# Performance work log

Measured on AMD Instinct MI355X. Metric: run time of the kernel, lower is better.

Reference implementation:

```python
import jax, jax.numpy as jnp
import numpy as np

ALPHA = 1.702   # GLU sigmoid scale
LIMIT = 7.0     # clamp limit
K = 2           # experts per token


def setup_inputs() -> dict:
    key = jax.random.key(0)
    ks = jax.random.split(key, 4)
    B, S, H, E, I = 1, 1024, 1024, 8, 1024
    return {
        "hidden_states": jax.random.normal(ks[0], (B, S, H), jnp.float32),
        "router_weight": jax.random.normal(ks[1], (E, H), jnp.float32),
        "router_bias": jnp.zeros((E,), jnp.float32),
        "gate_up_proj": jax.random.normal(ks[2], (E, H, 2 * I), jnp.float32) * 0.02,
        "gate_up_bias": jnp.zeros((E, 2 * I), jnp.float32),
        "down_proj": jax.random.normal(ks[3], (E, I, H), jnp.float32) * 0.02,
        "down_bias": jnp.zeros((E, H), jnp.float32),
    }


def reference(hidden_states, router_weight, router_bias, gate_up_proj,
              gate_up_bias, down_proj, down_bias):
    B, S, H = hidden_states.shape
    E = router_weight.shape[0]
    I = down_proj.shape[1]
    T = B * S

    flat = hidden_states.reshape(T, H)

    # Router: softmax over experts, top-K selection (weights NOT renormalized).
    logits = flat @ router_weight.T + router_bias               # [T, E]
    scores = jax.nn.softmax(logits, axis=-1)
    topk_vals, topk_idx = jax.lax.top_k(scores, K)              # [T, K]

    # Dense per-token expert weight matrix (equivalent of dispatch metadata +
    # combine * topk_weights in the tt pipeline); top-k indices are unique.
    w = jnp.zeros((T, E), scores.dtype).at[
        jnp.arange(T)[:, None], topk_idx].set(topk_vals)        # [T, E]

    # Expert MLP with clamped GLU (gpt-oss style).
    gu = jnp.einsum('th,ehf->tef', flat, gate_up_proj) + gate_up_bias  # [T,E,2I]
    gate = jnp.minimum(gu[..., :I], LIMIT)
    up = jnp.clip(gu[..., I:], -LIMIT, LIMIT)
    glu = gate * jax.nn.sigmoid(gate * ALPHA)
    act = (up + 1.0) * glu                                       # [T, E, I]

    down = jnp.einsum('tei,eih->teh', act, down_proj) + down_bias  # [T, E, H]

    # Weighted combine over selected experts.
    out = jnp.einsum('teh,te->th', down, w)
    return out.reshape(B, S, H)
```

## Files before the change

kernel.cpp:

```cpp
#include <hip/hip_runtime.h>
#include <hip/hip_bf16.h>


typedef unsigned short u16;
typedef __attribute__((ext_vector_type(8))) __bf16 bf16x8;
typedef __attribute__((ext_vector_type(4))) float f32x4;

#define T_TOK 1024
#define H_DIM 1024
#define E_NUM 8
#define I_DIM 1024
#define ALPHA 1.702f
#define LIMIT 7.0f
#define LSTR 72
#define DPART (2048 * 1024)

__device__ __forceinline__ u16 f2bf(float f) {
    unsigned u = __builtin_bit_cast(unsigned, f);
    u = (u + 0x7FFFu + ((u >> 16) & 1u)) >> 16;
    return (u16)u;
}

__device__ __forceinline__ f32x4 mfma16(bf16x8 a, bf16x8 b, f32x4 c) {
    return __builtin_amdgcn_mfma_f32_16x16x32_bf16(a, b, c, 0, 0, 0);
}

__global__ void k_zero(int* counts) {
    if (threadIdx.x < E_NUM) counts[threadIdx.x] = 0;
}

__global__ __launch_bounds__(256) void k_router(
    const float* __restrict__ x, const float* __restrict__ rw,
    const float* __restrict__ rb,
    int* __restrict__ counts, int* __restrict__ tk_e, int* __restrict__ tk_slot,
    float* __restrict__ tk_w, int* __restrict__ tok_list,
    float* __restrict__ w_list, u16* __restrict__ xb)
{
    const int t = blockIdx.x;
    const int tid = threadIdx.x;
    const float4 xv = *(const float4*)(x + (size_t)t * H_DIM + tid * 4);

    unsigned lo = (unsigned)f2bf(xv.x) | ((unsigned)f2bf(xv.y) << 16);
    unsigned hi = (unsigned)f2bf(xv.z) | ((unsigned)f2bf(xv.w) << 16);
    *(uint2*)(xb + (size_t)t * H_DIM + tid * 4) = make_uint2(lo, hi);

    float p[E_NUM];
#pragma unroll
    for (int e = 0; e < E_NUM; ++e) {
        const float4 wv = *(const float4*)(rw + e * H_DIM + tid * 4);
        p[e] = xv.x * wv.x + xv.y * wv.y + xv.z * wv.z + xv.w * wv.w;
    }
#pragma unroll
    for (int off = 32; off; off >>= 1) {
#pragma unroll
        for (int e = 0; e < E_NUM; ++e) p[e] += __shfl_down(p[e], off, 64);
    }
    __shared__ float red[4][E_NUM];
    const int lane = tid & 63, wvid = tid >> 6;
    if (lane == 0) {
#pragma unroll
        for (int e = 0; e < E_NUM; ++e) red[wvid][e] = p[e];
    }
    __syncthreads();
    if (tid == 0) {
        float lg[E_NUM];
#pragma unroll
        for (int e = 0; e < E_NUM; ++e)
            lg[e] = red[0][e] + red[1][e] + red[2][e] + red[3][e] + rb[e];
        float m1 = -1e30f, m2 = -1e30f; int i1 = 0, i2 = 0;
#pragma unroll
        for (int e = 0; e < E_NUM; ++e) {
            float l = lg[e];
            if (l > m1) { m2 = m1; i2 = i1; m1 = l; i1 = e; }
            else if (l > m2) { m2 = l; i2 = e; }
        }
        float s = 0.f;
#pragma unroll
        for (int e = 0; e < E_NUM; ++e) s += __expf(lg[e] - m1);
        const float w0 = 1.0f / s;
        const float w1 = __expf(m2 - m1) / s;
        int ee[2] = { i1, i2 };
        float ww[2] = { w0, w1 };
#pragma unroll
        for (int k = 0; k < 2; ++k) {
            int e = ee[k];
            int slot = atomicAdd(&counts[e], 1);
            tok_list[e * T_TOK + slot] = t;
            w_list[e * T_TOK + slot] = ww[k];
            tk_e[t * 2 + k] = e;
            tk_slot[t * 2 + k] = slot;
            tk_w[t * 2 + k] = ww[k];
        }
    }
}

__global__ void k_prefix(const int* __restrict__ counts, int* __restrict__ ebase) {
    if (threadIdx.x == 0) {
        int a = 0;
        for (int e = 0; e < E_NUM; ++e) { ebase[e] = a; a += counts[e]; }
    }
}

__global__ __launch_bounds__(256) void k_gateup(
    const float* __restrict__ gup, const float* __restrict__ gub,
    const int* __restrict__ counts, const int* __restrict__ ebase,
    const int* __restrict__ tok_list, const u16* __restrict__ xb,
    u16* __restrict__ act)
{
    const int e = blockIdx.z;
    const int cnt = counts[e];
    const int m0 = blockIdx.y * 64;
    if (m0 >= cnt) return;
    const int n0 = blockIdx.x * 32;
    const int abase = ebase[e];
    const int tid = threadIdx.x;

    __shared__ __align__(16) u16 As[64 * LSTR];
    __shared__ __align__(16) u16 Bs[64 * LSTR];

    const int arow_i = tid >> 2, akq = (tid & 3) * 16;
    const int aslot = m0 + arow_i;
    const int atok = (aslot < cnt) ? tok_list[e * T_TOK + aslot] : 0;
    const u16* asrc = xb + (size_t)atok * H_DIM + akq;
    u16* adst = &As[arow_i * LSTR + akq];

    const int kk = tid >> 2, q = tid & 3;
    const float* bg = gup + ((size_t)e << 21) + n0 + q * 4;
    const float* bu = bg + 1024;

    const int lane = tid & 63, wv = tid >> 6;
    const int fm = lane & 15, kg = lane >> 4;

    f32x4 accg[2], accu[2];
#pragma unroll
    for (int nt = 0; nt < 2; ++nt) {
        accg[nt] = (f32x4){0.f, 0.f, 0.f, 0.f};
        accu[nt] = (f32x4){0.f, 0.f, 0.f, 0.f};
    }

    uint4  pa0, pa1;
    float4 pg0, pg1, pu0, pu1;
    {
        pa0 = *(const uint4*)(asrc);
        pa1 = *(const uint4*)(asrc + 8);
        const float* g = bg + (size_t)kk * 2048;
        const float* u = bu + (size_t)kk * 2048;
        pg0 = *(const float4*)(g);      pg1 = *(const float4*)(g + 16);
        pu0 = *(const float4*)(u);      pu1 = *(const float4*)(u + 16);
    }

    for (int kb = 0; kb < H_DIM; kb += 64) {
        __syncthreads();
        *(uint4*)adst       = pa0;
        *(uint4*)(adst + 8) = pa1;
        {
            const float* g0 = (const float*)&pg0; const float* g1 = (const float*)&pg1;
            const float* u0 = (const float*)&pu0; const float* u1 = (const float*)&pu1;
#pragma unroll
            for (int j = 0; j < 4; ++j) {
                Bs[(q * 4 + j) * LSTR + kk]      = f2bf(g0[j]);
                Bs[(16 + q * 4 + j) * LSTR + kk] = f2bf(g1[j]);
                Bs[(32 + q * 4 + j) * LSTR + kk] = f2bf(u0[j]);
                Bs[(48 + q * 4 + j) * LSTR + kk] = f2bf(u1[j]);
            }
        }
        if (kb + 64 < H_DIM) {
            const u16* a = asrc + kb + 64;
            pa0 = *(const uint4*)(a);
            pa1 = *(const uint4*)(a + 8);
            const float* g = bg + (size_t)(kb + 64 + kk) * 2048;
            const float* u = bu + (size_t)(kb + 64 + kk) * 2048;
            pg0 = *(const float4*)(g);      pg1 = *(const float4*)(g + 16);
            pu0 = *(const float4*)(u);      pu1 = *(const float4*)(u + 16);
        }
        __syncthreads();

#pragma unroll
        for (int sub = 0; sub < 2; ++sub) {
            bf16x8 af = *(const bf16x8*)&As[(wv * 16 + fm) * LSTR + sub * 32 + kg * 8];
#pragma unroll
            for (int nt = 0; nt < 2; ++nt) {
                bf16x8 bgf = *(const bf16x8*)&Bs[(nt * 16 + fm) * LSTR + sub * 32 + kg * 8];
                bf16x8 buf = *(const bf16x8*)&Bs[(32 + nt * 16 + fm) * LSTR + sub * 32 + kg * 8];
                accg[nt] = mfma16(af, bgf, accg[nt]);
                accu[nt] = mfma16(af, buf, accu[nt]);
            }
        }
    }

#pragma unroll
    for (int r = 0; r < 4; ++r) {
        int rowb = wv * 16 + kg * 4 + r;
        int slot = m0 + rowb;
        if (slot >= cnt) continue;
        size_t arow_o = (size_t)(abase + slot) * I_DIM;
#pragma unroll
        for (int nt = 0; nt < 2; ++nt) {
            int cn = n0 + nt * 16 + fm;
            float g = accg[nt][r] + gub[e * 2048 + cn];
            float u = accu[nt][r] + gub[e * 2048 + 1024 + cn];
            g = fminf(g, LIMIT);
            u = fminf(fmaxf(u, -LIMIT), LIMIT);
            float glu = g / (1.f + __expf(-ALPHA * g));
            act[arow_o + cn] = f2bf((u + 1.f) * glu);
        }
    }
}

__global__ __launch_bounds__(256) void k_down(
    const float* __restrict__ dp,
    const int* __restrict__ counts, const int* __restrict__ ebase,
    const float* __restrict__ w_list,
    const u16* __restrict__ act, float* __restrict__ dout)
{
    const int e = blockIdx.z & 7, ks = blockIdx.z >> 3;
    const int cnt = counts[e];
    const int m0 = blockIdx.y * 64;
    if (m0 >= cnt) return;
    const int n0 = blockIdx.x * 64;
    const int abase = ebase[e];
    const int tid = threadIdx.x;

    __shared__ __align__(16) u16 As[64 * LSTR];
    __shared__ __align__(16) u16 Bs[64 * LSTR];

    const int arow_i = tid >> 2, akq = (tid & 3) * 16;
    const u16* asrc = act + (size_t)(abase + m0 + arow_i) * I_DIM + ks * 512 + akq;
    u16* adst = &As[arow_i * LSTR + akq];

    const int kk = tid >> 2, q = tid & 3;
    const float* bsrc = dp + ((size_t)e << 20) + (size_t)(ks * 512) * 1024 + n0 + q * 4;

    const int lane = tid & 63, wv = tid >> 6;
    const int fm = lane & 15, kg = lane >> 4;

    f32x4 acc[4];
#pragma unroll
    for (int nt = 0; nt < 4; ++nt) acc[nt] = (f32x4){0.f, 0.f, 0.f, 0.f};

    uint4  pa0, pa1;
    float4 pb0, pb1, pb2, pb3;
    {
        pa0 = *(const uint4*)(asrc);
        pa1 = *(const uint4*)(asrc + 8);
        const float* b = bsrc + (size_t)kk * 1024;
        pb0 = *(const float4*)(b);       pb1 = *(const float4*)(b + 16);
        pb2 = *(const float4*)(b + 32);  pb3 = *(const float4*)(b + 48);
    }

    for (int kb = 0; kb < 512; kb += 64) {
        __syncthreads();
        *(uint4*)adst       = pa0;
        *(uint4*)(adst + 8) = pa1;
        {
            const float* b0 = (const float*)&pb0; const float* b1 = (const float*)&pb1;
            const float* b2 = (const float*)&pb2; const float* b3 = (const float*)&pb3;
#pragma unroll
            for (int j = 0; j < 4; ++j) {
                Bs[(q * 4 + j) * LSTR + kk]      = f2bf(b0[j]);
                Bs[(16 + q * 4 + j) * LSTR + kk] = f2bf(b1[j]);
                Bs[(32 + q * 4 + j) * LSTR + kk] = f2bf(b2[j]);
                Bs[(48 + q * 4 + j) * LSTR + kk] = f2bf(b3[j]);
            }
        }
        if (kb + 64 < 512) {
            const u16* a = asrc + kb + 64;
            pa0 = *(const uint4*)(a);
            pa1 = *(const uint4*)(a + 8);
            const float* b = bsrc + (size_t)(kb + 64 + kk) * 1024;
            pb0 = *(const float4*)(b);       pb1 = *(const float4*)(b + 16);
            pb2 = *(const float4*)(b + 32);  pb3 = *(const float4*)(b + 48);
        }
        __syncthreads();

#pragma unroll
        for (int sub = 0; sub < 2; ++sub) {
            bf16x8 af = *(const bf16x8*)&As[(wv * 16 + fm) * LSTR + sub * 32 + kg * 8];
#pragma unroll
            for (int nt = 0; nt < 4; ++nt) {
                bf16x8 b = *(const bf16x8*)&Bs[(nt * 16 + fm) * LSTR + sub * 32 + kg * 8];
                acc[nt] = mfma16(af, b, acc[nt]);
            }
        }
    }

#pragma unroll
    for (int r = 0; r < 4; ++r) {
        int rowb = wv * 16 + kg * 4 + r;
        int slot = m0 + rowb;
        if (slot >= cnt) continue;
        float wgt = w_list[e * T_TOK + slot];
        size_t drow = (size_t)ks * DPART + (size_t)(abase + slot) * H_DIM;
#pragma unroll
        for (int nt = 0; nt < 4; ++nt)
            dout[drow + n0 + nt * 16 + fm] = acc[nt][r] * wgt;
    }
}

__global__ __launch_bounds__(256) void k_combine(
    const float* __restrict__ dout, const float* __restrict__ db,
    const int* __restrict__ tk_e, const int* __restrict__ tk_slot,
    const float* __restrict__ tk_w, const int* __restrict__ ebase,
    float* __restrict__ out)
{
    const int t = blockIdx.x, tid = threadIdx.x;
    const int e0 = tk_e[t * 2], e1 = tk_e[t * 2 + 1];
    const size_t p0 = (size_t)(ebase[e0] + tk_slot[t * 2]) * H_DIM;
    const size_t p1 = (size_t)(ebase[e1] + tk_slot[t * 2 + 1]) * H_DIM;
    const float w0 = tk_w[t * 2], w1 = tk_w[t * 2 + 1];
    const int c = tid * 4;
    float4 a0 = *(const float4*)(dout + p0 + c);
    float4 a1 = *(const float4*)(dout + DPART + p0 + c);
    float4 b0 = *(const float4*)(dout + p1 + c);
    float4 b1 = *(const float4*)(dout + DPART + p1 + c);
    float4 d0 = *(const float4*)(db + e0 * H_DIM + c);
    float4 d1 = *(const float4*)(db + e1 * H_DIM + c);
    float4 o;
    o.x = a0.x + a1.x + b0.x + b1.x + w0 * d0.x + w1 * d1.x;
    o.y = a0.y + a1.y + b0.y + b1.y + w0 * d0.y + w1 * d1.y;
    o.z = a0.z + a1.z + b0.z + b1.z + w0 * d0.z + w1 * d1.z;
    o.w = a0.w + a1.w + b0.w + b1.w + w0 * d0.w + w1 * d1.w;
    *(float4*)(out + (size_t)t * H_DIM + c) = o;
}

extern "C" void kernel_launch(void* const* d_in, const int* in_sizes, int n_in,
                              void* d_out, int out_size, void* d_ws, size_t ws_size,
                              hipStream_t stream) {
    const float* x   = (const float*)d_in[0];
    const float* rw  = (const float*)d_in[1];
    const float* rb  = (const float*)d_in[2];
    const float* gup = (const float*)d_in[3];
    const float* gub = (const float*)d_in[4];
    const float* dp  = (const float*)d_in[5];
    const float* db  = (const float*)d_in[6];
    float* out = (float*)d_out;

    char* ws = (char*)d_ws;
    int*   counts   = (int*)(ws);
    int*   ebase    = (int*)(ws + 32);
    int*   tk_e     = (int*)(ws + 64);
    int*   tk_slot  = (int*)(ws + 64 + 8192);
    float* tk_w     = (float*)(ws + 64 + 16384);
    int*   tok_list = (int*)(ws + 64 + 24576);
    float* w_list   = (float*)(ws + 64 + 24576 + 32768);
    u16*   xb       = (u16*)(ws + 90368);
    u16*   act      = (u16*)(ws + 90368 + 2097152);
    float* dout     = (float*)(ws + 90368 + 2097152 + 4456448);

    k_zero<<<1, 64, 0, stream>>>(counts);
    k_router<<<T_TOK, 256, 0, stream>>>(x, rw, rb, counts, tk_e, tk_slot, tk_w,
                                        tok_list, w_list, xb);
    k_prefix<<<1, 64, 0, stream>>>(counts, ebase);
    k_gateup<<<dim3(32, 16, 8), 256, 0, stream>>>(gup, gub, counts, ebase,
                                                  tok_list, xb, act);
    k_down<<<dim3(16, 16, 16), 256, 0, stream>>>(dp, counts, ebase, w_list, act, dout);
    k_combine<<<T_TOK, 256, 0, stream>>>(dout, db, tk_e, tk_slot, tk_w, ebase, out);
}
```

Baseline: 219.1 us.

## Fuse combine into down via atomics, drop prefix kernel, double-buffer loads

The router kernel now writes the weighted down-bias into the output. The down GEMM scatters weighted partial results straight into the output with float atomicAdd, so the split-K scratch buffer and the separate combine and prefix kernels are gone. Expert offsets are recomputed from counts inside each GEMM block. Weight staging now packs two k rows per 32-bit LDS store using a packed bf16 convert, and register prefetch is double-buffered two tiles ahead. The change trades two launches and a round-trip through the intermediate buffer for atomic contention and non-deterministic summation order.

```diff
diff --git a/kernel.cpp b/kernel.cpp
--- a/kernel.cpp
+++ b/kernel.cpp
@@ -13,7 +13,6 @@
 #define ALPHA 1.702f
 #define LIMIT 7.0f
 #define LSTR 72
-#define DPART (2048 * 1024)
 
 __device__ __forceinline__ u16 f2bf(float f) {
     unsigned u = __builtin_bit_cast(unsigned, f);
@@ -21,28 +20,49 @@
     return (u16)u;
 }
 
+__device__ __forceinline__ unsigned pk2(float lo, float hi) {
+#if defined(__has_builtin) && __has_builtin(__builtin_amdgcn_cvt_pk_bf16_f32)
+    typedef __attribute__((ext_vector_type(2))) __bf16 bf16x2_t;
+    bf16x2_t v = __builtin_amdgcn_cvt_pk_bf16_f32(lo, hi);
+    return __builtin_bit_cast(unsigned, v);
+#else
+    return (unsigned)f2bf(lo) | ((unsigned)f2bf(hi) << 16);
+#endif
+}
+
 __device__ __forceinline__ f32x4 mfma16(bf16x8 a, bf16x8 b, f32x4 c) {
     return __builtin_amdgcn_mfma_f32_16x16x32_bf16(a, b, c, 0, 0, 0);
 }
 
+__device__ __forceinline__ void expert_range(const int* counts, int e,
+                                             int& cnt, int& abase) {
+    int a = 0, c = 0;
+#pragma unroll
+    for (int i = 0; i < E_NUM; ++i) {
+        int v = counts[i];
+        if (i < e) a += v;
+        if (i == e) c = v;
+    }
+    cnt = c; abase = a;
+}
+
 __global__ void k_zero(int* counts) {
     if (threadIdx.x < E_NUM) counts[threadIdx.x] = 0;
 }
 
 __global__ __launch_bounds__(256) void k_router(
     const float* __restrict__ x, const float* __restrict__ rw,
-    const float* __restrict__ rb,
-    int* __restrict__ counts, int* __restrict__ tk_e, int* __restrict__ tk_slot,
-    float* __restrict__ tk_w, int* __restrict__ tok_list,
-    float* __restrict__ w_list, u16* __restrict__ xb)
+    const float* __restrict__ rb, const float* __restrict__ db,
+    int* __restrict__ counts, int* __restrict__ tok_list,
+    float* __restrict__ w_list, u16* __restrict__ xb,
+    float* __restrict__ out)
 {
     const int t = blockIdx.x;
     const int tid = threadIdx.x;
     const float4 xv = *(const float4*)(x + (size_t)t * H_DIM + tid * 4);
 
-    unsigned lo = (unsigned)f2bf(xv.x) | ((unsigned)f2bf(xv.y) << 16);
-    unsigned hi = (unsigned)f2bf(xv.z) | ((unsigned)f2bf(xv.w) << 16);
-    *(uint2*)(xb + (size_t)t * H_DIM + tid * 4) = make_uint2(lo, hi);
+    *(uint2*)(xb + (size_t)t * H_DIM + tid * 4) =
+        make_uint2(pk2(xv.x, xv.y), pk2(xv.z, xv.w));
 
     float p[E_NUM];
 #pragma unroll
@@ -56,6 +76,8 @@
         for (int e = 0; e < E_NUM; ++e) p[e] += __shfl_down(p[e], off, 64);
     }
     __shared__ float red[4][E_NUM];
+    __shared__ int se[2];
+    __shared__ float sw[2];
     const int lane = tid & 63, wvid = tid >> 6;
     if (lane == 0) {
 #pragma unroll
@@ -79,44 +101,44 @@
         for (int e = 0; e < E_NUM; ++e) s += __expf(lg[e] - m1);
         const float w0 = 1.0f / s;
         const float w1 = __expf(m2 - m1) / s;
-        int ee[2] = { i1, i2 };
-        float ww[2] = { w0, w1 };
-#pragma unroll
-        for (int k = 0; k < 2; ++k) {
-            int e = ee[k];
-            int slot = atomicAdd(&counts[e], 1);
-            tok_list[e * T_TOK + slot] = t;
-            w_list[e * T_TOK + slot] = ww[k];
-            tk_e[t * 2 + k] = e;
-            tk_slot[t * 2 + k] = slot;
-            tk_w[t * 2 + k] = ww[k];
-        }
-    }
-}
-
-__global__ void k_prefix(const int* __restrict__ counts, int* __restrict__ ebase) {
-    if (threadIdx.x == 0) {
-        int a = 0;
-        for (int e = 0; e < E_NUM; ++e) { ebase[e] = a; a += counts[e]; }
-    }
+        int slot0 = atomicAdd(&counts[i1], 1);
+        tok_list[i1 * T_TOK + slot0] = t;
+        w_list[i1 * T_TOK + slot0] = w0;
+        int slot1 = atomicAdd(&counts[i2], 1);
+        tok_list[i2 * T_TOK + slot1] = t;
+        w_list[i2 * T_TOK + slot1] = w1;
+        se[0] = i1; se[1] = i2; sw[0] = w0; sw[1] = w1;
+    }
+    __syncthreads();
+    const int e0 = se[0], e1 = se[1];
+    const float w0 = sw[0], w1 = sw[1];
+    const int c = tid * 4;
+    float4 d0 = *(const float4*)(db + e0 * H_DIM + c);
+    float4 d1 = *(const float4*)(db + e1 * H_DIM + c);
+    float4 o;
+    o.x = w0 * d0.x + w1 * d1.x;
+    o.y = w0 * d0.y + w1 * d1.y;
+    o.z = w0 * d0.z + w1 * d1.z;
+    o.w = w0 * d0.w + w1 * d1.w;
+    *(float4*)(out + (size_t)t * H_DIM + c) = o;
 }
 
 __global__ __launch_bounds__(256) void k_gateup(
     const float* __restrict__ gup, const float* __restrict__ gub,
-    const int* __restrict__ counts, const int* __restrict__ ebase,
-    const int* __restrict__ tok_list, const u16* __restrict__ xb,
-    u16* __restrict__ act)
+    const int* __restrict__ counts, const int* __restrict__ tok_list,
+    const u16* __restrict__ xb, u16* __restrict__ act)
 {
     const int e = blockIdx.z;
-    const int cnt = counts[e];
+    int cnt, abase;
+    expert_range(counts, e, cnt, abase);
     const int m0 = blockIdx.y * 64;
     if (m0 >= cnt) return;
     const int n0 = blockIdx.x * 32;
-    const int abase = ebase[e];
     const int tid = threadIdx.x;
 
     __shared__ __align__(16) u16 As[64 * LSTR];
     __shared__ __align__(16) u16 Bs[64 * LSTR];
+    unsigned* Bs32 = (unsigned*)Bs;
 
     const int arow_i = tid >> 2, akq = (tid & 3) * 16;
     const int aslot = m0 + arow_i;
@@ -124,9 +146,8 @@
     const u16* asrc = xb + (size_t)atok * H_DIM + akq;
     u16* adst = &As[arow_i * LSTR + akq];
 
-    const int kk = tid >> 2, q = tid & 3;
-    const float* bg = gup + ((size_t)e << 21) + n0 + q * 4;
-    const float* bu = bg + 1024;
+    const int kp = tid >> 3, q = tid & 7;
+    const float* bgate = gup + ((size_t)e << 21) + n0 + q * 4;
 
     const int lane = tid & 63, wv = tid >> 6;
     const int fm = lane & 15, kg = lane >> 4;
@@ -138,55 +159,65 @@
         accu[nt] = (f32x4){0.f, 0.f, 0.f, 0.f};
     }
 
-    uint4  pa0, pa1;
-    float4 pg0, pg1, pu0, pu1;
-    {
-        pa0 = *(const uint4*)(asrc);
-        pa1 = *(const uint4*)(asrc + 8);
-        const float* g = bg + (size_t)kk * 2048;
-        const float* u = bu + (size_t)kk * 2048;
-        pg0 = *(const float4*)(g);      pg1 = *(const float4*)(g + 16);
-        pu0 = *(const float4*)(u);      pu1 = *(const float4*)(u + 16);
-    }
-
-    for (int kb = 0; kb < H_DIM; kb += 64) {
-        __syncthreads();
-        *(uint4*)adst       = pa0;
-        *(uint4*)(adst + 8) = pa1;
-        {
-            const float* g0 = (const float*)&pg0; const float* g1 = (const float*)&pg1;
-            const float* u0 = (const float*)&pu0; const float* u1 = (const float*)&pu1;
-#pragma unroll
-            for (int j = 0; j < 4; ++j) {
-                Bs[(q * 4 + j) * LSTR + kk]      = f2bf(g0[j]);
-                Bs[(16 + q * 4 + j) * LSTR + kk] = f2bf(g1[j]);
-                Bs[(32 + q * 4 + j) * LSTR + kk] = f2bf(u0[j]);
-                Bs[(48 + q * 4 + j) * LSTR + kk] = f2bf(u1[j]);
-            }
-        }
-        if (kb + 64 < H_DIM) {
-            const u16* a = asrc + kb + 64;
-            pa0 = *(const uint4*)(a);
-            pa1 = *(const uint4*)(a + 8);
-            const float* g = bg + (size_t)(kb + 64 + kk) * 2048;
-            const float* u = bu + (size_t)(kb + 64 + kk) * 2048;
-            pg0 = *(const float4*)(g);      pg1 = *(const float4*)(g + 16);
-            pu0 = *(const float4*)(u);      pu1 = *(const float4*)(u + 16);
-        }
-        __syncthreads();
-
-#pragma unroll
-        for (int sub = 0; sub < 2; ++sub) {
-            bf16x8 af = *(const bf16x8*)&As[(wv * 16 + fm) * LSTR + sub * 32 + kg * 8];
-#pragma unroll
-            for (int nt = 0; nt < 2; ++nt) {
-                bf16x8 bgf = *(const bf16x8*)&Bs[(nt * 16 + fm) * LSTR + sub * 32 + kg * 8];
-                bf16x8 buf = *(const bf16x8*)&Bs[(32 + nt * 16 + fm) * LSTR + sub * 32 + kg * 8];
-                accg[nt] = mfma16(af, bgf, accg[nt]);
-                accu[nt] = mfma16(af, buf, accu[nt]);
-            }
-        }
-    }
+#define GU_LOAD(A0, A1, G0, G1, U0, U1, KB)                                    \
+    {                                                                          \
+        const u16* ap_ = asrc + (KB);                                          \
+        A0 = *(const uint4*)(ap_);                                             \
+        A1 = *(const uint4*)(ap_ + 8);                                         \
+        const float* gp_ = bgate + (size_t)((KB) + 2 * kp) * 2048;             \
+        G0 = *(const float4*)(gp_);                                            \
+        G1 = *(const float4*)(gp_ + 2048);                                     \
+        U0 = *(const float4*)(gp_ + 1024);                                     \
+        U1 = *(const float4*)(gp_ + 3072);                                     \
+    }
+#define GU_STORE(A0, A1, G0, G1, U0, U1)                                       \
+    {                                                                          \
+        *(uint4*)adst       = A0;                                              \
+        *(uint4*)(adst + 8) = A1;                                              \
+        const float* g0_ = (const float*)&G0; const float* g1_ = (const float*)&G1; \
+        const float* u0_ = (const float*)&U0; const float* u1_ = (const float*)&U1; \
+        _Pragma("unroll")                                                      \
+        for (int j = 0; j < 4; ++j) {                                          \
+            Bs32[(q * 4 + j) * 36 + kp]        = pk2(g0_[j], g1_[j]);          \
+            Bs32[(32 + q * 4 + j) * 36 + kp]   = pk2(u0_[j], u1_[j]);          \
+        }                                                                      \
+    }
+#define GU_MFMA()                                                              \
+    {                                                                          \
+        _Pragma("unroll")                                                      \
+        for (int sub = 0; sub < 2; ++sub) {                                    \
+            bf16x8 af = *(const bf16x8*)&As[(wv * 16 + fm) * LSTR + sub * 32 + kg * 8]; \
+            _Pragma("unroll")                                                  \
+            for (int nt = 0; nt < 2; ++nt) {                                   \
+                bf16x8 bg = *(const bf16x8*)&Bs[(nt * 16 + fm) * LSTR + sub * 32 + kg * 8]; \
+                bf16x8 bu = *(const bf16x8*)&Bs[(32 + nt * 16 + fm) * LSTR + sub * 32 + kg * 8]; \
+                accg[nt] = mfma16(af, bg, accg[nt]);                           \
+                accu[nt] = mfma16(af, bu, accu[nt]);                           \
+            }                                                                  \
+        }                                                                      \
+    }
+
+    uint4 a0s0, a1s0, a0s1, a1s1;
+    float4 g0s0, g1s0, u0s0, u1s0, g0s1, g1s1, u0s1, u1s1;
+    GU_LOAD(a0s0, a1s0, g0s0, g1s0, u0s0, u1s0, 0);
+    GU_LOAD(a0s1, a1s1, g0s1, g1s1, u0s1, u1s1, 64);
+
+    for (int kb = 0; kb < H_DIM; kb += 128) {
+        __syncthreads();
+        GU_STORE(a0s0, a1s0, g0s0, g1s0, u0s0, u1s0);
+        if (kb + 128 < H_DIM) GU_LOAD(a0s0, a1s0, g0s0, g1s0, u0s0, u1s0, kb + 128);
+        __syncthreads();
+        GU_MFMA();
+
+        __syncthreads();
+        GU_STORE(a0s1, a1s1, g0s1, g1s1, u0s1, u1s1);
+        if (kb + 192 < H_DIM) GU_LOAD(a0s1, a1s1, g0s1, g1s1, u0s1, u1s1, kb + 192);
+        __syncthreads();
+        GU_MFMA();
+    }
+#undef GU_LOAD
+#undef GU_STORE
+#undef GU_MFMA
 
 #pragma unroll
     for (int r = 0; r < 4; ++r) {
@@ -209,26 +240,27 @@
 
 __global__ __launch_bounds__(256) void k_down(
     const float* __restrict__ dp,
-    const int* __restrict__ counts, const int* __restrict__ ebase,
+    const int* __restrict__ counts, const int* __restrict__ tok_list,
     const float* __restrict__ w_list,
-    const u16* __restrict__ act, float* __restrict__ dout)
+    const u16* __restrict__ act, float* __restrict__ out)
 {
     const int e = blockIdx.z & 7, ks = blockIdx.z >> 3;
-    const int cnt = counts[e];
+    int cnt, abase;
+    expert_range(counts, e, cnt, abase);
     const int m0 = blockIdx.y * 64;
     if (m0 >= cnt) return;
     const int n0 = blockIdx.x * 64;
-    const int abase = ebase[e];
     const int tid = threadIdx.x;
 
     __shared__ __align__(16) u16 As[64 * LSTR];
     __shared__ __align__(16) u16 Bs[64 * LSTR];
+    unsigned* Bs32 = (unsigned*)Bs;
 
     const int arow_i = tid >> 2, akq = (tid & 3) * 16;
     const u16* asrc = act + (size_t)(abase + m0 + arow_i) * I_DIM + ks * 512 + akq;
     u16* adst = &As[arow_i * LSTR + akq];
 
-    const int kk = tid >> 2, q = tid & 3;
+    const int kp = tid >> 3, q = tid & 7;
     const float* bsrc = dp + ((size_t)e << 20) + (size_t)(ks * 512) * 1024 + n0 + q * 4;
 
     const int lane = tid & 63, wv = tid >> 6;
@@ -238,51 +270,63 @@
 #pragma unroll
     for (int nt = 0; nt < 4; ++nt) acc[nt] = (f32x4){0.f, 0.f, 0.f, 0.f};
 
-    uint4  pa0, pa1;
-    float4 pb0, pb1, pb2, pb3;
-    {
-        pa0 = *(const uint4*)(asrc);
-        pa1 = *(const uint4*)(asrc + 8);
-        const float* b = bsrc + (size_t)kk * 1024;
-        pb0 = *(const float4*)(b);       pb1 = *(const float4*)(b + 16);
-        pb2 = *(const float4*)(b + 32);  pb3 = *(const float4*)(b + 48);
-    }
-
-    for (int kb = 0; kb < 512; kb += 64) {
-        __syncthreads();
-        *(uint4*)adst       = pa0;
-        *(uint4*)(adst + 8) = pa1;
-        {
-            const float* b0 = (const float*)&pb0; const float* b1 = (const float*)&pb1;
-            const float* b2 = (const float*)&pb2; const float* b3 = (const float*)&pb3;
-#pragma unroll
-            for (int j = 0; j < 4; ++j) {
-                Bs[(q * 4 + j) * LSTR + kk]      = f2bf(b0[j]);
-                Bs[(16 + q * 4 + j) * LSTR + kk] = f2bf(b1[j]);
-                Bs[(32 + q * 4 + j) * LSTR + kk] = f2bf(b2[j]);
-                Bs[(48 + q * 4 + j) * LSTR + kk] = f2bf(b3[j]);
-            }
-        }
-        if (kb + 64 < 512) {
-            const u16* a = asrc + kb + 64;
-            pa0 = *(const uint4*)(a);
-            pa1 = *(const uint4*)(a + 8);
-            const float* b = bsrc + (size_t)(kb + 64 + kk) * 1024;
-            pb0 = *(const float4*)(b);       pb1 = *(const float4*)(b + 16);
-            pb2 = *(const float4*)(b + 32);  pb3 = *(const float4*)(b + 48);
-        }
-        __syncthreads();
-
-#pragma unroll
-        for (int sub = 0; sub < 2; ++sub) {
-            bf16x8 af = *(const bf16x8*)&As[(wv * 16 + fm) * LSTR + sub * 32 + kg * 8];
-#pragma unroll
-            for (int nt = 0; nt < 4; ++nt) {
-                bf16x8 b = *(const bf16x8*)&Bs[(nt * 16 + fm) * LSTR + sub * 32 + kg * 8];
-                acc[nt] = mfma16(af, b, acc[nt]);
-            }
-        }
-    }
+#define DN_LOAD(A0, A1, B00, B01, B10, B11, KB)                                \
+    {                                                                          \
+        const u16* ap_ = asrc + (KB);                                          \
+        A0 = *(const uint4*)(ap_);                                             \
+        A1 = *(const uint4*)(ap_ + 8);                                         \
+        const float* bp_ = bsrc + (size_t)((KB) + 2 * kp) * 1024;              \
+        B00 = *(const float4*)(bp_);                                           \
+        B01 = *(const float4*)(bp_ + 1024);                                    \
+        B10 = *(const float4*)(bp_ + 32);                                      \
+        B11 = *(const float4*)(bp_ + 1056);                                    \
+    }
+#define DN_STORE(A0, A1, B00, B01, B10, B11)                                   \
+    {                                                                          \
+        *(uint4*)adst       = A0;                                              \
+        *(uint4*)(adst + 8) = A1;                                              \
+        const float* b00_ = (const float*)&B00; const float* b01_ = (const float*)&B01; \
+        const float* b10_ = (const float*)&B10; const float* b11_ = (const float*)&B11; \
+        _Pragma("unroll")                                                      \
+        for (int j = 0; j < 4; ++j) {                                          \
+            Bs32[(q * 4 + j) * 36 + kp]      = pk2(b00_[j], b01_[j]);          \
+            Bs32[(32 + q * 4 + j) * 36 + kp] = pk2(b10_[j], b11_[j]);          \
+        }                                                                      \
+    }
+#define DN_MFMA()                                                              \
+    {                                                                          \
+        _Pragma("unroll")                                                      \
+        for (int sub = 0; sub < 2; ++sub) {                                    \
+            bf16x8 af = *(const bf16x8*)&As[(wv * 16 + fm) * LSTR + sub * 32 + kg * 8]; \
+            _Pragma("unroll")                                                  \
+            for (int nt = 0; nt < 4; ++nt) {                                   \
+                bf16x8 b = *(const bf16x8*)&Bs[(nt * 16 + fm) * LSTR + sub * 32 + kg * 8]; \
+                acc[nt] = mfma16(af, b, acc[nt]);                              \
+            }                                                                  \
+        }                                                                      \
+    }
+
+    uint4 a0s0, a1s0, a0s1, a1s1;
+    float4 b00s0, b01s0, b10s0, b11s0, b00s1, b01s1, b10s1, b11s1;
+    DN_LOAD(a0s0, a1s0, b00s0, b01s0, b10s0, b11s0, 0);
+    DN_LOAD(a0s1, a1s1, b00s1, b01s1, b10s1, b11s1, 64);
+
+    for (int kb = 0; kb < 512; kb += 128) {
+        __syncthreads();
+        DN_STORE(a0s0, a1s0, b00s0, b01s0, b10s0, b11s0);
+        if (kb + 128 < 512) DN_LOAD(a0s0, a1s0, b00s0, b01s0, b10s0, b11s0, kb + 128);
+        __syncthreads();
+        DN_MFMA();
+
+        __syncthreads();
+        DN_STORE(a0s1, a1s1, b00s1, b01s1, b10s1, b11s1);
+        if (kb + 192 < 512) DN_LOAD(a0s1, a1s1, b00s1, b01s1, b10s1, b11s1, kb + 192);
+        __syncthreads();
+        DN_MFMA();
+    }
+#undef DN_LOAD
+#undef DN_STORE
+#undef DN_MFMA
 
 #pragma unroll
     for (int r = 0; r < 4; ++r) {
@@ -290,37 +334,12 @@
         int slot = m0 + rowb;
         if (slot >= cnt) continue;
         float wgt = w_list[e * T_TOK + slot];
-        size_t drow = (size_t)ks * DPART + (size_t)(abase + slot) * H_DIM;
+        int tok = tok_list[e * T_TOK + slot];
+        float* orow = out + (size_t)tok * H_DIM + n0;
 #pragma unroll
         for (int nt = 0; nt < 4; ++nt)
-            dout[drow + n0 + nt * 16 + fm] = acc[nt][r] * wgt;
-    }
-}
-
-__global__ __launch_bounds__(256) void k_combine(
-    const float* __restrict__ dout, const float* __restrict__ db,
-    const int* __restrict__ tk_e, const int* __restrict__ tk_slot,
-    const float* __restrict__ tk_w, const int* __restrict__ ebase,
-    float* __restrict__ out)
-{
-    const int t = blockIdx.x, tid = threadIdx.x;
-    const int e0 = tk_e[t * 2], e1 = tk_e[t * 2 + 1];
-    const size_t p0 = (size_t)(ebase[e0] + tk_slot[t * 2]) * H_DIM;
-    const size_t p1 = (size_t)(ebase[e1] + tk_slot[t * 2 + 1]) * H_DIM;
-    const float w0 = tk_w[t * 2], w1 = tk_w[t * 2 + 1];
-    const int c = tid * 4;
-    float4 a0 = *(const float4*)(dout + p0 + c);
-    float4 a1 = *(const float4*)(dout + DPART + p0 + c);
-    float4 b0 = *(const float4*)(dout + p1 + c);
-    float4 b1 = *(const float4*)(dout + DPART + p1 + c);
-    float4 d0 = *(const float4*)(db + e0 * H_DIM + c);
-    float4 d1 = *(const float4*)(db + e1 * H_DIM + c);
-    float4 o;
-    o.x = a0.x + a1.x + b0.x + b1.x + w0 * d0.x + w1 * d1.x;
-    o.y = a0.y + a1.y + b0.y + b1.y + w0 * d0.y + w1 * d1.y;
-    o.z = a0.z + a1.z + b0.z + b1.z + w0 * d0.z + w1 * d1.z;
-    o.w = a0.w + a1.w + b0.w + b1.w + w0 * d0.w + w1 * d1.w;
-    *(float4*)(out + (size_t)t * H_DIM + c) = o;
+            atomicAdd(orow + nt * 16 + fm, acc[nt][r] * wgt);
+    }
 }
 
 extern "C" void kernel_launch(void* const* d_in, const int* in_sizes, int n_in,
@@ -337,22 +356,16 @@
 
     char* ws = (char*)d_ws;
     int*   counts   = (int*)(ws);
-    int*   ebase    = (int*)(ws + 32);
-    int*   tk_e     = (int*)(ws + 64);
-    int*   tk_slot  = (int*)(ws + 64 + 8192);
-    float* tk_w     = (float*)(ws + 64 + 16384);
-    int*   tok_list = (int*)(ws + 64 + 24576);
-    float* w_list   = (float*)(ws + 64 + 24576 + 32768);
-    u16*   xb       = (u16*)(ws + 90368);
-    u16*   act      = (u16*)(ws + 90368 + 2097152);
-    float* dout     = (float*)(ws + 90368 + 2097152 + 4456448);
+    int*   tok_list = (int*)(ws + 64);
+    float* w_list   = (float*)(ws + 64 + 32768);
+    u16*   xb       = (u16*)(ws + 65600);
+    u16*   act      = (u16*)(ws + 65600 + 2097152);
 
     k_zero<<<1, 64, 0, stream>>>(counts);
-    k_router<<<T_TOK, 256, 0, stream>>>(x, rw, rb, counts, tk_e, tk_slot, tk_w,
-                                        tok_list, w_list, xb);
-    k_prefix<<<1, 64, 0, stream>>>(counts, ebase);
-    k_gateup<<<dim3(32, 16, 8), 256, 0, stream>>>(gup, gub, counts, ebase,
-                                                  tok_list, xb, act);
-    k_down<<<dim3(16, 16, 16), 256, 0, stream>>>(dp, counts, ebase, w_list, act, dout);
-    k_combine<<<T_TOK, 256, 0, stream>>>(dout, db, tk_e, tk_slot, tk_w, ebase, out);
-}
+    k_router<<<T_TOK, 256, 0, stream>>>(x, rw, rb, db, counts, tok_list, w_list,
+                                        xb, out);
+    k_gateup<<<dim3(32, 16, 8), 256, 0, stream>>>(gup, gub, counts, tok_list,
+                                                  xb, act);
+    k_down<<<dim3(16, 16, 16), 256, 0, stream>>>(dp, counts, tok_list, w_list,
+                                                 act, out);
+}
```

Measured after the change: 212.0 us. 3.2% less time.
